# Optimization experiments

Measured on AMD Instinct MI355X. Metric: run time of the kernel, lower is better.

## Reference

```python
import jax, jax.numpy as jnp
import numpy as np

B, A, E, H = 512, 4, 10, 256
OBS, PHY, G, MV = 2, 3, 3, 2
T = 10
STEP = 0.05


def setup_inputs() -> dict:
    key = jax.random.key(0)
    ks = jax.random.split(key, 16)
    rn = lambda k, s, sc=1.0: jax.random.normal(k, s, jnp.float32) * sc
    W = 0.1  # weight scale so tanh/sigmoid stay in sane range
    return {
        'observations': rn(ks[0], (B, A, E, OBS)),
        'physical': rn(ks[1], (B, E, PHY)),
        'observed_goals': rn(ks[2], (B, A, G)),
        'mem_physical': jnp.zeros((B, A, E, H), jnp.float32),
        'mem_action': jnp.zeros((B, A, H), jnp.float32),
        'W_ih_p': rn(ks[3], (3 * H, OBS + PHY), W),
        'W_hh_p': rn(ks[4], (3 * H, H), W),
        'b_ih_p': jnp.zeros((3 * H,), jnp.float32),
        'b_hh_p': jnp.zeros((3 * H,), jnp.float32),
        'W_fc_p': rn(ks[5], (H, H), W),
        'b_fc_p': jnp.zeros((H,), jnp.float32),
        'W_ih_a': rn(ks[6], (3 * H, H + G), W),
        'W_hh_a': rn(ks[7], (3 * H, H), W),
        'b_ih_a': jnp.zeros((3 * H,), jnp.float32),
        'b_hh_a': jnp.zeros((3 * H,), jnp.float32),
        'W_fc_a': rn(ks[8], (H, H), W),
        'b_fc_a': jnp.zeros((H,), jnp.float32),
        'W_m1': rn(ks[9], (H, H), W),
        'b_m1': jnp.zeros((H,), jnp.float32),
        'W_m2': rn(ks[10], (MV, H), W),
        'b_m2': jnp.zeros((MV,), jnp.float32),
    }


def _gru(x, h, Wih, Whh, bih, bhh):
    # torch.nn.GRUCell math, vectorized over leading dims
    gi = x @ Wih.T + bih
    gh = h @ Whh.T + bhh
    ir, iz, inn = jnp.split(gi, 3, axis=-1)
    hr, hz, hn = jnp.split(gh, 3, axis=-1)
    r = jax.nn.sigmoid(ir + hr)
    z = jax.nn.sigmoid(iz + hz)
    n = jnp.tanh(inn + r * hn)
    return (1.0 - z) * n + z * h


def reference(observations, physical, observed_goals, mem_physical, mem_action,
              W_ih_p, W_hh_p, b_ih_p, b_hh_p, W_fc_p, b_fc_p,
              W_ih_a, W_hh_a, b_ih_a, b_hh_a, W_fc_a, b_fc_a,
              W_m1, b_m1, W_m2, b_m2):
    b, a, e, _ = observations.shape
    # per-(agent, entity) input: cat(observation, entity physical features)
    phys_b = jnp.broadcast_to(physical[:, None], (b, a, e, physical.shape[-1]))
    x_p = jnp.concatenate([observations, phys_b], axis=-1)  # [B,A,E,5]

    def step(carry, _):
        mp, ma = carry  # [B,A,E,H], [B,A,H]
        # physical ProcessingModule over all (agent, entity) pairs at once
        h_p = _gru(x_p, mp, W_ih_p, W_hh_p, b_ih_p, b_hh_p)          # new 'physical' memory
        proc = jax.nn.elu(h_p @ W_fc_p.T + b_fc_p)                    # [B,A,E,H]
        feat = jnp.max(proc, axis=2)                                  # AdaptiveMaxPool2d((1,H)) over entities
        # ActionModule: GRU over cat(pooled physical feat, observed goal)
        x_a = jnp.concatenate([feat, observed_goals], axis=-1)       # [B,A,H+G]
        h_a = _gru(x_a, ma, W_ih_a, W_hh_a, b_ih_a, b_hh_a)          # new 'action' memory
        proc_a = jax.nn.elu(h_a @ W_fc_a.T + b_fc_a)
        mv = jnp.tanh(jax.nn.elu(proc_a @ W_m1.T + b_m1) @ W_m2.T + b_m2) * STEP  # [B,A,MV]
        return (h_p, h_a), mv

    _, movements = jax.lax.scan(step, (mem_physical, mem_action), None, length=T)
    return movements  # [T,B,A,MV]
```

## Files before the change

kernel.cpp:

```cpp
#include <hip/hip_runtime.h>
#include <math.h>

#define H 256
#define G3 768
#define BB 512
#define AA 4
#define EE 10
#define RP (BB*AA*EE)
#define RA (BB*AA)
#define TT 10
#define NMV 2
#define STEPSC 0.05f
#define DST 260
#define A1B 128
#define A2B 256
#define A3B 128
#define COMB 1280

typedef __attribute__((ext_vector_type(8))) short short8;
typedef __attribute__((ext_vector_type(8))) _Float16 half8;
typedef __attribute__((ext_vector_type(4))) _Float16 half4;
typedef __attribute__((ext_vector_type(4))) float f32x4;

#if defined(__has_builtin)
#  if __has_builtin(__builtin_amdgcn_global_load_lds)
#    define HAS_GLL 1
#  endif
#endif

__device__ __forceinline__ float sigmoid_(float x){ return 1.f/(1.f + __expf(-x)); }
__device__ __forceinline__ float tanh_(float x){
    float ax = fabsf(x);
    float e  = __expf(-2.f*ax);
    float t  = (1.f - e)/(1.f + e);
    return copysignf(t, x);
}
__device__ __forceinline__ float elu_(float x){ return x > 0.f ? x : (__expf(x) - 1.f); }

#define MFMA16(A,B,C) __builtin_amdgcn_mfma_f32_16x16x32_f16(A,B,C,0,0,0)

__device__ __forceinline__ void cp16(const void* g, void* l) {
#ifdef HAS_GLL
    __builtin_amdgcn_global_load_lds(
        (const __attribute__((address_space(1))) unsigned int*)g,
        (__attribute__((address_space(3))) unsigned int*)l, 16, 0, 0);
#else
    *(short8*)l = *(const short8*)g;
#endif
}

__global__ void k_splitw(const float* __restrict__ src, _Float16* __restrict__ dst,
                         int n, int ldsrc)
{
    int i = blockIdx.x*256 + threadIdx.x;
    if (i < n) {
        int j  = i & 7;
        int l  = (i >> 3) & 63;
        int kc = (i >> 9) & 7;
        int c  = i >> 12;
        int row = c*16 + (l & 15);
        int k   = kc*32 + (l >> 4)*8 + j;
        dst[i] = (_Float16)src[(size_t)row*ldsrc + k];
    }
}

__global__ void k_gia_goal(const float* __restrict__ goals,
                           const float* __restrict__ Wiha,
                           const float* __restrict__ biha,
                           const float* __restrict__ bhha,
                           _Float16* __restrict__ out)
{
    int idx = blockIdx.x*256 + threadIdx.x;
    int ra = idx / G3, k = idx % G3;
    float g0 = goals[ra*3+0], g1 = goals[ra*3+1], g2 = goals[ra*3+2];
    const float* w = Wiha + (size_t)k*259 + 256;
    float base = biha[k] + (k < 512 ? bhha[k] : 0.f);
    out[idx] = (_Float16)(base + g0*w[0] + g1*w[1] + g2*w[2]);
}

__global__ void k_cvt(const float* __restrict__ src, _Float16* __restrict__ dst, int n)
{
    int i = blockIdx.x*256 + threadIdx.x;
    if (i < n) dst[i] = (_Float16)src[i];
}

__global__ void k_xext(const float* __restrict__ obs, const float* __restrict__ phys,
                       _Float16* __restrict__ dst)
{
    int i = blockIdx.x*256 + threadIdx.x;
    int row = i >> 5, j = i & 31;
    float v = 0.f;
    if (j < 2) v = obs[(size_t)row*2 + j];
    else if (j < 5) {
        int bb = row / (AA*EE), e = row % EE;
        v = phys[(size_t)(bb*EE + e)*3 + (j - 2)];
    } else if (j == 5) v = 1.f;
    dst[i] = (_Float16)v;
}

__global__ void k_wxih(const float* __restrict__ Wih, const float* __restrict__ bih,
                       const float* __restrict__ bhh, _Float16* __restrict__ dst)
{
    int i = blockIdx.x*256 + threadIdx.x;
    int j = i & 7, l = (i >> 3) & 63, chunk = i >> 9;
    int g = chunk >> 4, cs = chunk & 15;
    int ocol = g*256 + cs*16 + (l & 15);
    int k32 = (l >> 4)*8 + j;
    float v = 0.f;
    if (k32 < 5) v = Wih[(size_t)ocol*5 + k32];
    else if (k32 == 5) v = bih[ocol] + (g < 2 ? bhh[ocol] : 0.f);
    dst[i] = (_Float16)v;
}

__global__ __launch_bounds__(256, 2)
void k_step(int gru_t, int fc_t, int a1_t, int a2_t, int a3_t,
            _Float16* __restrict__ hp0, _Float16* __restrict__ hp1,
            _Float16* __restrict__ proc0, _Float16* __restrict__ proc1,
            _Float16* __restrict__ ha0, _Float16* __restrict__ ha1,
            _Float16* __restrict__ pca0, _Float16* __restrict__ pca1,
            const _Float16* __restrict__ wWhh, const _Float16* __restrict__ wWfc,
            const _Float16* __restrict__ wWhha, const _Float16* __restrict__ wWiha,
            const _Float16* __restrict__ wWfca, const _Float16* __restrict__ wWm1,
            const _Float16* __restrict__ gia,
            const _Float16* __restrict__ xext, const _Float16* __restrict__ wXih,
            const float* __restrict__ bhh, const float* __restrict__ bfcp,
            const float* __restrict__ bhha, const float* __restrict__ bfca,
            const float* __restrict__ bm1,
            const float* __restrict__ Wm2, const float* __restrict__ bm2,
            float* __restrict__ out)
{
    __shared__ char smem[24576];
    int b = blockIdx.x;
    const int tid = threadIdx.x;
    const int wv = tid >> 6, lane = tid & 63;
    const int quad = lane >> 4, l16 = lane & 15;

    if (b < A1B) {
        if (a1_t < 0) return;
        float* D = (float*)smem;
        const _Float16* proc = (a1_t & 1) ? proc1 : proc0;
        const _Float16* hain = (a1_t & 1) ? ha1 : ha0;
        _Float16*      haout = (a1_t & 1) ? ha0 : ha1;
        const int ra0 = b*16;

        for (int i = tid; i < 16*32; i += 256) {
            int r = i >> 5, cg = (i & 31)*8;
            const _Float16* p = proc + ((size_t)(ra0 + r)*EE)*H + cg;
            half8 v = *(const half8*)p;
            float m[8];
            #pragma unroll
            for (int j = 0; j < 8; j++) m[j] = (float)v[j];
            #pragma unroll
            for (int e = 1; e < EE; e++) {
                half8 u = *(const half8*)(p + (size_t)e*H);
                #pragma unroll
                for (int j = 0; j < 8; j++) m[j] = fmaxf(m[j], (float)u[j]);
            }
            #pragma unroll
            for (int j = 0; j < 8; j++) D[r*DST + cg + j] = m[j];
        }
        __syncthreads();

        half8 Fh[8], Hh[8];
        #pragma unroll
        for (int kc = 0; kc < 8; kc++) {
            const float* fp = &D[l16*DST + quad*8 + kc*32];
            #pragma unroll
            for (int j = 0; j < 8; j++) Fh[kc][j] = (_Float16)fp[j];
            Hh[kc] = *(const half8*)(hain + (size_t)(ra0 + l16)*H + quad*8 + kc*32);
        }

        const int smp = ra0 + l16;
        const _Float16* gp = gia + (size_t)smp*G3;
        #pragma unroll
        for (int p = 0; p < 2; p++) {
            f32x4 gh[3][2], gx[3][2];
            #pragma unroll
            for (int g = 0; g < 3; g++)
                #pragma unroll
                for (int ch = 0; ch < 2; ch++) {
                    gh[g][ch] = (f32x4){0.f,0.f,0.f,0.f};
                    gx[g][ch] = (f32x4){0.f,0.f,0.f,0.f};
                }
            #pragma unroll
            for (int kc = 0; kc < 8; kc++)
                #pragma unroll
                for (int ch = 0; ch < 2; ch++)
                    #pragma unroll
                    for (int g = 0; g < 3; g++) {
                        const size_t cg = (size_t)(g*16 + wv*4 + p*2 + ch);
                        half8 bh = *(const half8*)(wWhha + (cg*8+kc)*512 + lane*8);
                        half8 bx = *(const half8*)(wWiha + (cg*8+kc)*512 + lane*8);
                        gh[g][ch] = MFMA16(bh, Hh[kc], gh[g][ch]);
                        gx[g][ch] = MFMA16(bx, Fh[kc], gx[g][ch]);
                    }
            #pragma unroll
            for (int ch = 0; ch < 2; ch++) {
                const int c0 = (wv*4 + p*2 + ch)*16 + quad*4;
                half4 gr4 = *(const half4*)(gp + c0);
                half4 gz4 = *(const half4*)(gp + 256 + c0);
                half4 gn4 = *(const half4*)(gp + 512 + c0);
                f32x4 bn4 = *(const f32x4*)&bhha[512 + c0];
                half4 hp4 = *(const half4*)(hain + (size_t)smp*H + c0);
                half4 ho;
                #pragma unroll
                for (int r = 0; r < 4; r++) {
                    float rg = sigmoid_((float)gr4[r] + gx[0][ch][r] + gh[0][ch][r]);
                    float z  = sigmoid_((float)gz4[r] + gx[1][ch][r] + gh[1][ch][r]);
                    float n  = tanh_((float)gn4[r] + gx[2][ch][r] + rg*(gh[2][ch][r] + bn4[r]));
                    ho[r] = (_Float16)((1.f - z)*n + z*(float)hp4[r]);
                }
                *(half4*)(haout + (size_t)smp*H + c0) = ho;
            }
        }
        return;
    }
    b -= A1B;

    if (b < A2B) {
        if (a2_t < 0) return;
        const _Float16* hnew = (a2_t & 1) ? ha0 : ha1;
        _Float16*       pca  = (a2_t & 1) ? pca1 : pca0;
        const int ra0 = (b >> 1)*16;
        const int half = b & 1;

        half8 Hh[8];
        #pragma unroll
        for (int kc = 0; kc < 8; kc++)
            Hh[kc] = *(const half8*)(hnew + (size_t)(ra0 + l16)*H + quad*8 + kc*32);

        f32x4 ac[2];
        ac[0] = (f32x4){0.f,0.f,0.f,0.f};
        ac[1] = (f32x4){0.f,0.f,0.f,0.f};
        #pragma unroll
        for (int kc = 0; kc < 8; kc++)
            #pragma unroll
            for (int ch = 0; ch < 2; ch++) {
                const size_t cidx = (size_t)(half*8 + wv*2 + ch);
                half8 w = *(const half8*)(wWfca + (cidx*8+kc)*512 + lane*8);
                ac[ch] = MFMA16(w, Hh[kc], ac[ch]);
            }
        const int smp = ra0 + l16;
        #pragma unroll
        for (int ch = 0; ch < 2; ch++) {
            const int c0 = (half*8 + wv*2 + ch)*16 + quad*4;
            f32x4 bs4 = *(const f32x4*)&bfca[c0];
            half4 po;
            #pragma unroll
            for (int r = 0; r < 4; r++)
                po[r] = (_Float16)elu_(ac[ch][r] + bs4[r]);
            *(half4*)(pca + (size_t)smp*H + c0) = po;
        }
        return;
    }
    b -= A2B;

    if (b < A3B) {
        if (a3_t < 0) return;
        float* D = (float*)smem;
        const _Float16* pca = (a3_t & 1) ? pca1 : pca0;
        const int ra0 = b*16;

        half8 Ph[8];
        #pragma unroll
        for (int kc = 0; kc < 8; kc++)
            Ph[kc] = *(const half8*)(pca + (size_t)(ra0 + l16)*H + quad*8 + kc*32);

        f32x4 ac[4];
        #pragma unroll
        for (int ch = 0; ch < 4; ch++) ac[ch] = (f32x4){0.f,0.f,0.f,0.f};
        #pragma unroll
        for (int kc = 0; kc < 8; kc++)
            #pragma unroll
            for (int ch = 0; ch < 4; ch++) {
                half8 w = *(const half8*)(wWm1 + ((size_t)(wv*4+ch)*8+kc)*512 + lane*8);
                ac[ch] = MFMA16(w, Ph[kc], ac[ch]);
            }
        #pragma unroll
        for (int ch = 0; ch < 4; ch++) {
            const int c0 = (wv*4 + ch)*16 + quad*4;
            f32x4 bs4 = *(const f32x4*)&bm1[c0];
            f32x4 dv;
            #pragma unroll
            for (int r = 0; r < 4; r++) dv[r] = elu_(ac[ch][r] + bs4[r]);
            *(f32x4*)&D[l16*DST + c0] = dv;
        }
        __syncthreads();

        if (tid < 32) {
            int r = tid >> 1, v = tid & 1;
            const float* w = Wm2 + (size_t)v*H;
            float s = bm2[v];
            #pragma unroll 4
            for (int i = 0; i < H/4; i++) {
                float4 a = *(const float4*)&D[r*DST + i*4];
                float4 c = *(const float4*)&w[i*4];
                s = fmaf(a.x,c.x,s); s = fmaf(a.y,c.y,s);
                s = fmaf(a.z,c.z,s); s = fmaf(a.w,c.w,s);
            }
            out[((size_t)a3_t*RA + ra0 + r)*NMV + v] = tanh_(s)*STEPSC;
        }
        return;
    }
    b -= A3B;

    {
        const bool do_gru = (gru_t >= 0);
        const bool do_fc  = (fc_t >= 0);
        if (!do_gru && !do_fc) return;
        _Float16* Bw = (_Float16*)smem;
        const int par = do_gru ? (gru_t & 1) : ((fc_t + 1) & 1);
        const _Float16* hin  = par ? hp1 : hp0;
        _Float16*       hout = par ? hp0 : hp1;
        _Float16*       pout = (fc_t & 1) ? proc1 : proc0;
        const int xm = b % 160, ys = b / 160;
        const int mt0 = xm*128 + wv*16;
        const int mt1 = mt0 + 64;

        half8 Ah[2][8];
        #pragma unroll
        for (int kc = 0; kc < 8; kc++) {
            Ah[0][kc] = *(const half8*)(hin + (size_t)(mt0 + l16)*H + quad*8 + kc*32);
            Ah[1][kc] = *(const half8*)(hin + (size_t)(mt1 + l16)*H + quad*8 + kc*32);
        }

        if (do_gru) {
            half8 Xh[2];
            Xh[0] = *(const half8*)(xext + (size_t)(mt0 + l16)*32 + quad*8);
            Xh[1] = *(const half8*)(xext + (size_t)(mt1 + l16)*32 + quad*8);

            for (int s = 0; s < 2; s++) {
                const int cs = ys*2 + s;
                if (s) __syncthreads();
                #pragma unroll
                for (int k = 0; k < 6; k++) {
                    int i = tid + 256*k;
                    int g = i >> 9;
                    cp16(wWhh + (size_t)(g*16+cs)*4096 + (i & 511)*8, &Bw[(size_t)i*8]);
                }
                __syncthreads();

                f32x4 acc[2][3], accHN[2];
                #pragma unroll
                for (int mt = 0; mt < 2; mt++) {
                    #pragma unroll
                    for (int g = 0; g < 3; g++) acc[mt][g] = (f32x4){0.f,0.f,0.f,0.f};
                    accHN[mt] = (f32x4){0.f,0.f,0.f,0.f};
                }
                #pragma unroll
                for (int kc = 0; kc < 8; kc++) {
                    #pragma unroll
                    for (int g = 0; g < 2; g++) {
                        half8 w = *(const half8*)&Bw[(g*8 + kc)*512 + lane*8];
                        acc[0][g] = MFMA16(w, Ah[0][kc], acc[0][g]);
                        acc[1][g] = MFMA16(w, Ah[1][kc], acc[1][g]);
                    }
                    half8 wn = *(const half8*)&Bw[(2*8 + kc)*512 + lane*8];
                    accHN[0] = MFMA16(wn, Ah[0][kc], accHN[0]);
                    accHN[1] = MFMA16(wn, Ah[1][kc], accHN[1]);
                }
                #pragma unroll
                for (int g = 0; g < 3; g++) {
                    half8 xw = *(const half8*)(wXih + (size_t)(g*16+cs)*512 + lane*8);
                    acc[0][g] = MFMA16(xw, Xh[0], acc[0][g]);
                    acc[1][g] = MFMA16(xw, Xh[1], acc[1][g]);
                }

                const int c0 = cs*16 + quad*4;
                f32x4 bn4 = *(const f32x4*)&bhh[512 + c0];
                #pragma unroll
                for (int mt = 0; mt < 2; mt++) {
                    const int smp = (mt ? mt1 : mt0) + l16;
                    half4 hp4 = *(const half4*)(hin + (size_t)smp*H + c0);
                    half4 ho;
                    #pragma unroll
                    for (int r = 0; r < 4; r++) {
                        float rg = sigmoid_(acc[mt][0][r]);
                        float z  = sigmoid_(acc[mt][1][r]);
                        float n  = tanh_(acc[mt][2][r] + rg*(accHN[mt][r] + bn4[r]));
                        ho[r] = (_Float16)((1.f - z)*n + z*(float)hp4[r]);
                    }
                    *(half4*)(hout + (size_t)smp*H + c0) = ho;
                }
            }
        }

        if (do_fc) {
            const int cs2 = ys;
            __syncthreads();
            #pragma unroll
            for (int k = 0; k < 4; k++) {
                int i = tid + 256*k;
                cp16(wWfc + (size_t)cs2*8192 + i*8, &Bw[(size_t)i*8]);
            }
            __syncthreads();

            f32x4 acc[2][2];
            #pragma unroll
            for (int mt = 0; mt < 2; mt++)
                #pragma unroll
                for (int ni = 0; ni < 2; ni++) acc[mt][ni] = (f32x4){0.f,0.f,0.f,0.f};
            #pragma unroll
            for (int kc = 0; kc < 8; kc++)
                #pragma unroll
                for (int ni = 0; ni < 2; ni++) {
                    half8 w = *(const half8*)&Bw[ni*4096 + kc*512 + lane*8];
                    acc[0][ni] = MFMA16(w, Ah[0][kc], acc[0][ni]);
                    acc[1][ni] = MFMA16(w, Ah[1][kc], acc[1][ni]);
                }
            #pragma unroll
            for (int ni = 0; ni < 2; ni++) {
                const int c0 = cs2*32 + ni*16 + quad*4;
                f32x4 bs4 = *(const f32x4*)&bfcp[c0];
                #pragma unroll
                for (int mt = 0; mt < 2; mt++) {
                    const int smp = (mt ? mt1 : mt0) + l16;
                    half4 po;
                    #pragma unroll
                    for (int r = 0; r < 4; r++)
                        po[r] = (_Float16)elu_(acc[mt][ni][r] + bs4[r]);
                    *(half4*)(pout + (size_t)smp*H + c0) = po;
                }
            }
        }
    }
}

extern "C" void kernel_launch(void* const* d_in, const int* in_sizes, int n_in,
                              void* d_out, int out_size, void* d_ws, size_t ws_size,
                              hipStream_t stream)
{
    const float* obs  = (const float*)d_in[0];
    const float* phys = (const float*)d_in[1];
    const float* goals= (const float*)d_in[2];
    const float* memp = (const float*)d_in[3];
    const float* mema = (const float*)d_in[4];
    const float* Wihp = (const float*)d_in[5];
    const float* Whhp = (const float*)d_in[6];
    const float* bihp = (const float*)d_in[7];
    const float* bhhp = (const float*)d_in[8];
    const float* Wfcp = (const float*)d_in[9];
    const float* bfcp = (const float*)d_in[10];
    const float* Wiha = (const float*)d_in[11];
    const float* Whha = (const float*)d_in[12];
    const float* biha = (const float*)d_in[13];
    const float* bhha = (const float*)d_in[14];
    const float* Wfca = (const float*)d_in[15];
    const float* bfca = (const float*)d_in[16];
    const float* Wm1  = (const float*)d_in[17];
    const float* bm1  = (const float*)d_in[18];
    const float* Wm2  = (const float*)d_in[19];
    const float* bm2  = (const float*)d_in[20];
    float* out = (float*)d_out;
    (void)ws_size;

    char* base = (char*)d_ws;
    size_t off = 0;
    auto alloc = [&](size_t bytes) -> char* {
        char* p = base + off;
        off += (bytes + 255) & ~(size_t)255;
        return p;
    };
    _Float16* wp_whh = (_Float16*)alloc((size_t)G3*H*2);
    _Float16* wp_wfc = (_Float16*)alloc((size_t)H*H*2);
    _Float16* wa_whh = (_Float16*)alloc((size_t)G3*H*2);
    _Float16* wa_wih = (_Float16*)alloc((size_t)G3*H*2);
    _Float16* wa_wfc = (_Float16*)alloc((size_t)H*H*2);
    _Float16* wa_wm1 = (_Float16*)alloc((size_t)H*H*2);
    _Float16* gia    = (_Float16*)alloc((size_t)RA*G3*2);
    _Float16* hp0    = (_Float16*)alloc((size_t)RP*H*2);
    _Float16* hp1    = (_Float16*)alloc((size_t)RP*H*2);
    _Float16* proc0  = (_Float16*)alloc((size_t)RP*H*2);
    _Float16* proc1  = (_Float16*)alloc((size_t)RP*H*2);
    _Float16* ha0    = (_Float16*)alloc((size_t)RA*H*2);
    _Float16* ha1    = (_Float16*)alloc((size_t)RA*H*2);
    _Float16* pca0   = (_Float16*)alloc((size_t)RA*H*2);
    _Float16* pca1   = (_Float16*)alloc((size_t)RA*H*2);
    _Float16* xext   = (_Float16*)alloc((size_t)RP*32*2);
    _Float16* wxih   = (_Float16*)alloc((size_t)48*512*2);

    k_splitw<<<(G3*H+255)/256, 256, 0, stream>>>(Whhp, wp_whh, G3*H, H);
    k_splitw<<<(H*H+255)/256, 256, 0, stream>>>(Wfcp, wp_wfc, H*H, H);
    k_splitw<<<(G3*H+255)/256, 256, 0, stream>>>(Whha, wa_whh, G3*H, H);
    k_splitw<<<(G3*H+255)/256, 256, 0, stream>>>(Wiha, wa_wih, G3*H, 259);
    k_splitw<<<(H*H+255)/256, 256, 0, stream>>>(Wfca, wa_wfc, H*H, H);
    k_splitw<<<(H*H+255)/256, 256, 0, stream>>>(Wm1,  wa_wm1, H*H, H);
    k_gia_goal<<<RA*G3/256, 256, 0, stream>>>(goals, Wiha, biha, bhha, gia);
    k_cvt<<<((size_t)RP*H+255)/256, 256, 0, stream>>>(memp, hp0, RP*H);
    k_cvt<<<((size_t)RA*H+255)/256, 256, 0, stream>>>(mema, ha0, RA*H);
    k_xext<<<RP*32/256, 256, 0, stream>>>(obs, phys, xext);
    k_wxih<<<48*512/256, 256, 0, stream>>>(Wihp, bihp, bhhp, wxih);

    const int NB = A1B + A2B + A3B + COMB;
    for (int L = 0; L <= TT + 3; L++) {
        int gru_t = (L <= TT-1) ? L : -1;
        int fc_t  = (L-1 >= 0 && L-1 <= TT-1) ? L-1 : -1;
        int a1_t  = (L-2 >= 0 && L-2 <= TT-1) ? L-2 : -1;
        int a2_t  = (L-3 >= 0 && L-3 <= TT-1) ? L-3 : -1;
        int a3_t  = (L-4 >= 0 && L-4 <= TT-1) ? L-4 : -1;
        k_step<<<NB, 256, 0, stream>>>(gru_t, fc_t, a1_t, a2_t, a3_t,
                                       hp0, hp1, proc0, proc1, ha0, ha1, pca0, pca1,
                                       wp_whh, wp_wfc, wa_whh, wa_wih, wa_wfc, wa_wm1,
                                       gia, xext, wxih,
                                       bhhp, bfcp,
                                       bhha, bfca, bm1, Wm2, bm2, out);
    }
}
```

Baseline: 599.0 us.

## Read GRU/FC weights straight from global memory and schedule heavy blocks first

The combined physical GRU+FC blocks no longer stage weight tiles into LDS with global_load_lds and barriers. Each wave now loads its MFMA B-fragments directly from global memory, relying on L1/L2 caching. Those heavy COMB blocks also move to the front of the grid so they dispatch before the lighter action-module blocks, and the shared memory size shrinks. The trade-off is more redundant global/L2 traffic per wave in exchange for removing the copy and sync overhead and possibly improving occupancy.

```diff
diff --git a/kernel.cpp b/kernel.cpp
--- a/kernel.cpp
+++ b/kernel.cpp
@@ -22,12 +22,6 @@
 typedef __attribute__((ext_vector_type(4))) _Float16 half4;
 typedef __attribute__((ext_vector_type(4))) float f32x4;
 
-#if defined(__has_builtin)
-#  if __has_builtin(__builtin_amdgcn_global_load_lds)
-#    define HAS_GLL 1
-#  endif
-#endif
-
 __device__ __forceinline__ float sigmoid_(float x){ return 1.f/(1.f + __expf(-x)); }
 __device__ __forceinline__ float tanh_(float x){
     float ax = fabsf(x);
@@ -38,16 +32,6 @@
 __device__ __forceinline__ float elu_(float x){ return x > 0.f ? x : (__expf(x) - 1.f); }
 
 #define MFMA16(A,B,C) __builtin_amdgcn_mfma_f32_16x16x32_f16(A,B,C,0,0,0)
-
-__device__ __forceinline__ void cp16(const void* g, void* l) {
-#ifdef HAS_GLL
-    __builtin_amdgcn_global_load_lds(
-        (const __attribute__((address_space(1))) unsigned int*)g,
-        (__attribute__((address_space(3))) unsigned int*)l, 16, 0, 0);
-#else
-    *(short8*)l = *(const short8*)g;
-#endif
-}
 
 __global__ void k_splitw(const float* __restrict__ src, _Float16* __restrict__ dst,
                          int n, int ldsrc)
@@ -129,186 +113,16 @@
             const float* __restrict__ Wm2, const float* __restrict__ bm2,
             float* __restrict__ out)
 {
-    __shared__ char smem[24576];
+    __shared__ char smem[16640];
     int b = blockIdx.x;
     const int tid = threadIdx.x;
     const int wv = tid >> 6, lane = tid & 63;
     const int quad = lane >> 4, l16 = lane & 15;
 
-    if (b < A1B) {
-        if (a1_t < 0) return;
-        float* D = (float*)smem;
-        const _Float16* proc = (a1_t & 1) ? proc1 : proc0;
-        const _Float16* hain = (a1_t & 1) ? ha1 : ha0;
-        _Float16*      haout = (a1_t & 1) ? ha0 : ha1;
-        const int ra0 = b*16;
-
-        for (int i = tid; i < 16*32; i += 256) {
-            int r = i >> 5, cg = (i & 31)*8;
-            const _Float16* p = proc + ((size_t)(ra0 + r)*EE)*H + cg;
-            half8 v = *(const half8*)p;
-            float m[8];
-            #pragma unroll
-            for (int j = 0; j < 8; j++) m[j] = (float)v[j];
-            #pragma unroll
-            for (int e = 1; e < EE; e++) {
-                half8 u = *(const half8*)(p + (size_t)e*H);
-                #pragma unroll
-                for (int j = 0; j < 8; j++) m[j] = fmaxf(m[j], (float)u[j]);
-            }
-            #pragma unroll
-            for (int j = 0; j < 8; j++) D[r*DST + cg + j] = m[j];
-        }
-        __syncthreads();
-
-        half8 Fh[8], Hh[8];
-        #pragma unroll
-        for (int kc = 0; kc < 8; kc++) {
-            const float* fp = &D[l16*DST + quad*8 + kc*32];
-            #pragma unroll
-            for (int j = 0; j < 8; j++) Fh[kc][j] = (_Float16)fp[j];
-            Hh[kc] = *(const half8*)(hain + (size_t)(ra0 + l16)*H + quad*8 + kc*32);
-        }
-
-        const int smp = ra0 + l16;
-        const _Float16* gp = gia + (size_t)smp*G3;
-        #pragma unroll
-        for (int p = 0; p < 2; p++) {
-            f32x4 gh[3][2], gx[3][2];
-            #pragma unroll
-            for (int g = 0; g < 3; g++)
-                #pragma unroll
-                for (int ch = 0; ch < 2; ch++) {
-                    gh[g][ch] = (f32x4){0.f,0.f,0.f,0.f};
-                    gx[g][ch] = (f32x4){0.f,0.f,0.f,0.f};
-                }
-            #pragma unroll
-            for (int kc = 0; kc < 8; kc++)
-                #pragma unroll
-                for (int ch = 0; ch < 2; ch++)
-                    #pragma unroll
-                    for (int g = 0; g < 3; g++) {
-                        const size_t cg = (size_t)(g*16 + wv*4 + p*2 + ch);
-                        half8 bh = *(const half8*)(wWhha + (cg*8+kc)*512 + lane*8);
-                        half8 bx = *(const half8*)(wWiha + (cg*8+kc)*512 + lane*8);
-                        gh[g][ch] = MFMA16(bh, Hh[kc], gh[g][ch]);
-                        gx[g][ch] = MFMA16(bx, Fh[kc], gx[g][ch]);
-                    }
-            #pragma unroll
-            for (int ch = 0; ch < 2; ch++) {
-                const int c0 = (wv*4 + p*2 + ch)*16 + quad*4;
-                half4 gr4 = *(const half4*)(gp + c0);
-                half4 gz4 = *(const half4*)(gp + 256 + c0);
-                half4 gn4 = *(const half4*)(gp + 512 + c0);
-                f32x4 bn4 = *(const f32x4*)&bhha[512 + c0];
-                half4 hp4 = *(const half4*)(hain + (size_t)smp*H + c0);
-                half4 ho;
-                #pragma unroll
-                for (int r = 0; r < 4; r++) {
-                    float rg = sigmoid_((float)gr4[r] + gx[0][ch][r] + gh[0][ch][r]);
-                    float z  = sigmoid_((float)gz4[r] + gx[1][ch][r] + gh[1][ch][r]);
-                    float n  = tanh_((float)gn4[r] + gx[2][ch][r] + rg*(gh[2][ch][r] + bn4[r]));
-                    ho[r] = (_Float16)((1.f - z)*n + z*(float)hp4[r]);
-                }
-                *(half4*)(haout + (size_t)smp*H + c0) = ho;
-            }
-        }
-        return;
-    }
-    b -= A1B;
-
-    if (b < A2B) {
-        if (a2_t < 0) return;
-        const _Float16* hnew = (a2_t & 1) ? ha0 : ha1;
-        _Float16*       pca  = (a2_t & 1) ? pca1 : pca0;
-        const int ra0 = (b >> 1)*16;
-        const int half = b & 1;
-
-        half8 Hh[8];
-        #pragma unroll
-        for (int kc = 0; kc < 8; kc++)
-            Hh[kc] = *(const half8*)(hnew + (size_t)(ra0 + l16)*H + quad*8 + kc*32);
-
-        f32x4 ac[2];
-        ac[0] = (f32x4){0.f,0.f,0.f,0.f};
-        ac[1] = (f32x4){0.f,0.f,0.f,0.f};
-        #pragma unroll
-        for (int kc = 0; kc < 8; kc++)
-            #pragma unroll
-            for (int ch = 0; ch < 2; ch++) {
-                const size_t cidx = (size_t)(half*8 + wv*2 + ch);
-                half8 w = *(const half8*)(wWfca + (cidx*8+kc)*512 + lane*8);
-                ac[ch] = MFMA16(w, Hh[kc], ac[ch]);
-            }
-        const int smp = ra0 + l16;
-        #pragma unroll
-        for (int ch = 0; ch < 2; ch++) {
-            const int c0 = (half*8 + wv*2 + ch)*16 + quad*4;
-            f32x4 bs4 = *(const f32x4*)&bfca[c0];
-            half4 po;
-            #pragma unroll
-            for (int r = 0; r < 4; r++)
-                po[r] = (_Float16)elu_(ac[ch][r] + bs4[r]);
-            *(half4*)(pca + (size_t)smp*H + c0) = po;
-        }
-        return;
-    }
-    b -= A2B;
-
-    if (b < A3B) {
-        if (a3_t < 0) return;
-        float* D = (float*)smem;
-        const _Float16* pca = (a3_t & 1) ? pca1 : pca0;
-        const int ra0 = b*16;
-
-        half8 Ph[8];
-        #pragma unroll
-        for (int kc = 0; kc < 8; kc++)
-            Ph[kc] = *(const half8*)(pca + (size_t)(ra0 + l16)*H + quad*8 + kc*32);
-
-        f32x4 ac[4];
-        #pragma unroll
-        for (int ch = 0; ch < 4; ch++) ac[ch] = (f32x4){0.f,0.f,0.f,0.f};
-        #pragma unroll
-        for (int kc = 0; kc < 8; kc++)
-            #pragma unroll
-            for (int ch = 0; ch < 4; ch++) {
-                half8 w = *(const half8*)(wWm1 + ((size_t)(wv*4+ch)*8+kc)*512 + lane*8);
-                ac[ch] = MFMA16(w, Ph[kc], ac[ch]);
-            }
-        #pragma unroll
-        for (int ch = 0; ch < 4; ch++) {
-            const int c0 = (wv*4 + ch)*16 + quad*4;
-            f32x4 bs4 = *(const f32x4*)&bm1[c0];
-            f32x4 dv;
-            #pragma unroll
-            for (int r = 0; r < 4; r++) dv[r] = elu_(ac[ch][r] + bs4[r]);
-            *(f32x4*)&D[l16*DST + c0] = dv;
-        }
-        __syncthreads();
-
-        if (tid < 32) {
-            int r = tid >> 1, v = tid & 1;
-            const float* w = Wm2 + (size_t)v*H;
-            float s = bm2[v];
-            #pragma unroll 4
-            for (int i = 0; i < H/4; i++) {
-                float4 a = *(const float4*)&D[r*DST + i*4];
-                float4 c = *(const float4*)&w[i*4];
-                s = fmaf(a.x,c.x,s); s = fmaf(a.y,c.y,s);
-                s = fmaf(a.z,c.z,s); s = fmaf(a.w,c.w,s);
-            }
-            out[((size_t)a3_t*RA + ra0 + r)*NMV + v] = tanh_(s)*STEPSC;
-        }
-        return;
-    }
-    b -= A3B;
-
-    {
+    if (b < COMB) {
         const bool do_gru = (gru_t >= 0);
         const bool do_fc  = (fc_t >= 0);
         if (!do_gru && !do_fc) return;
-        _Float16* Bw = (_Float16*)smem;
         const int par = do_gru ? (gru_t & 1) : ((fc_t + 1) & 1);
         const _Float16* hin  = par ? hp1 : hp0;
         _Float16*       hout = par ? hp0 : hp1;
@@ -329,16 +143,10 @@
             Xh[0] = *(const half8*)(xext + (size_t)(mt0 + l16)*32 + quad*8);
             Xh[1] = *(const half8*)(xext + (size_t)(mt1 + l16)*32 + quad*8);
 
+            #pragma unroll
             for (int s = 0; s < 2; s++) {
                 const int cs = ys*2 + s;
-                if (s) __syncthreads();
-                #pragma unroll
-                for (int k = 0; k < 6; k++) {
-                    int i = tid + 256*k;
-                    int g = i >> 9;
-                    cp16(wWhh + (size_t)(g*16+cs)*4096 + (i & 511)*8, &Bw[(size_t)i*8]);
-                }
-                __syncthreads();
+                const _Float16* wb = wWhh + (size_t)cs*4096 + (size_t)lane*8;
 
                 f32x4 acc[2][3], accHN[2];
                 #pragma unroll
@@ -351,11 +159,11 @@
                 for (int kc = 0; kc < 8; kc++) {
                     #pragma unroll
                     for (int g = 0; g < 2; g++) {
-                        half8 w = *(const half8*)&Bw[(g*8 + kc)*512 + lane*8];
+                        half8 w = *(const half8*)(wb + (size_t)g*65536 + kc*512);
                         acc[0][g] = MFMA16(w, Ah[0][kc], acc[0][g]);
                         acc[1][g] = MFMA16(w, Ah[1][kc], acc[1][g]);
                     }
-                    half8 wn = *(const half8*)&Bw[(2*8 + kc)*512 + lane*8];
+                    half8 wn = *(const half8*)(wb + (size_t)2*65536 + kc*512);
                     accHN[0] = MFMA16(wn, Ah[0][kc], accHN[0]);
                     accHN[1] = MFMA16(wn, Ah[1][kc], accHN[1]);
                 }
@@ -387,14 +195,7 @@
 
         if (do_fc) {
             const int cs2 = ys;
-            __syncthreads();
-            #pragma unroll
-            for (int k = 0; k < 4; k++) {
-                int i = tid + 256*k;
-                cp16(wWfc + (size_t)cs2*8192 + i*8, &Bw[(size_t)i*8]);
-            }
-            __syncthreads();
-
+            const _Float16* wf = wWfc + (size_t)cs2*8192 + (size_t)lane*8;
             f32x4 acc[2][2];
             #pragma unroll
             for (int mt = 0; mt < 2; mt++)
@@ -404,7 +205,7 @@
             for (int kc = 0; kc < 8; kc++)
                 #pragma unroll
                 for (int ni = 0; ni < 2; ni++) {
-                    half8 w = *(const half8*)&Bw[ni*4096 + kc*512 + lane*8];
+                    half8 w = *(const half8*)(wf + ni*4096 + kc*512);
                     acc[0][ni] = MFMA16(w, Ah[0][kc], acc[0][ni]);
                     acc[1][ni] = MFMA16(w, Ah[1][kc], acc[1][ni]);
                 }
@@ -423,6 +224,176 @@
                 }
             }
         }
+        return;
+    }
+    b -= COMB;
+
+    if (b < A1B) {
+        if (a1_t < 0) return;
+        float* D = (float*)smem;
+        const _Float16* proc = (a1_t & 1) ? proc1 : proc0;
+        const _Float16* hain = (a1_t & 1) ? ha1 : ha0;
+        _Float16*      haout = (a1_t & 1) ? ha0 : ha1;
+        const int ra0 = b*16;
+
+        for (int i = tid; i < 16*32; i += 256) {
+            int r = i >> 5, cg = (i & 31)*8;
+            const _Float16* p = proc + ((size_t)(ra0 + r)*EE)*H + cg;
+            half8 v = *(const half8*)p;
+            float m[8];
+            #pragma unroll
+            for (int j = 0; j < 8; j++) m[j] = (float)v[j];
+            #pragma unroll
+            for (int e = 1; e < EE; e++) {
+                half8 u = *(const half8*)(p + (size_t)e*H);
+                #pragma unroll
+                for (int j = 0; j < 8; j++) m[j] = fmaxf(m[j], (float)u[j]);
+            }
+            #pragma unroll
+            for (int j = 0; j < 8; j++) D[r*DST + cg + j] = m[j];
+        }
+        __syncthreads();
+
+        half8 Fh[8], Hh[8];
+        #pragma unroll
+        for (int kc = 0; kc < 8; kc++) {
+            const float* fp = &D[l16*DST + quad*8 + kc*32];
+            #pragma unroll
+            for (int j = 0; j < 8; j++) Fh[kc][j] = (_Float16)fp[j];
+            Hh[kc] = *(const half8*)(hain + (size_t)(ra0 + l16)*H + quad*8 + kc*32);
+        }
+
+        const int smp = ra0 + l16;
+        const _Float16* gp = gia + (size_t)smp*G3;
+        #pragma unroll
+        for (int p = 0; p < 2; p++) {
+            f32x4 gh[3][2], gx[3][2];
+            #pragma unroll
+            for (int g = 0; g < 3; g++)
+                #pragma unroll
+                for (int ch = 0; ch < 2; ch++) {
+                    gh[g][ch] = (f32x4){0.f,0.f,0.f,0.f};
+                    gx[g][ch] = (f32x4){0.f,0.f,0.f,0.f};
+                }
+            #pragma unroll
+            for (int kc = 0; kc < 8; kc++)
+                #pragma unroll
+                for (int ch = 0; ch < 2; ch++)
+                    #pragma unroll
+                    for (int g = 0; g < 3; g++) {
+                        const size_t cg = (size_t)(g*16 + wv*4 + p*2 + ch);
+                        half8 bh = *(const half8*)(wWhha + (cg*8+kc)*512 + lane*8);
+                        half8 bx = *(const half8*)(wWiha + (cg*8+kc)*512 + lane*8);
+                        gh[g][ch] = MFMA16(bh, Hh[kc], gh[g][ch]);
+                        gx[g][ch] = MFMA16(bx, Fh[kc], gx[g][ch]);
+                    }
+            #pragma unroll
+            for (int ch = 0; ch < 2; ch++) {
+                const int c0 = (wv*4 + p*2 + ch)*16 + quad*4;
+                half4 gr4 = *(const half4*)(gp + c0);
+                half4 gz4 = *(const half4*)(gp + 256 + c0);
+                half4 gn4 = *(const half4*)(gp + 512 + c0);
+                f32x4 bn4 = *(const f32x4*)&bhha[512 + c0];
+                half4 hp4 = *(const half4*)(hain + (size_t)smp*H + c0);
+                half4 ho;
+                #pragma unroll
+                for (int r = 0; r < 4; r++) {
+                    float rg = sigmoid_((float)gr4[r] + gx[0][ch][r] + gh[0][ch][r]);
+                    float z  = sigmoid_((float)gz4[r] + gx[1][ch][r] + gh[1][ch][r]);
+                    float n  = tanh_((float)gn4[r] + gx[2][ch][r] + rg*(gh[2][ch][r] + bn4[r]));
+                    ho[r] = (_Float16)((1.f - z)*n + z*(float)hp4[r]);
+                }
+                *(half4*)(haout + (size_t)smp*H + c0) = ho;
+            }
+        }
+        return;
+    }
+    b -= A1B;
+
+    if (b < A2B) {
+        if (a2_t < 0) return;
+        const _Float16* hnew = (a2_t & 1) ? ha0 : ha1;
+        _Float16*       pca  = (a2_t & 1) ? pca1 : pca0;
+        const int ra0 = (b >> 1)*16;
+        const int half = b & 1;
+
+        half8 Hh[8];
+        #pragma unroll
+        for (int kc = 0; kc < 8; kc++)
+            Hh[kc] = *(const half8*)(hnew + (size_t)(ra0 + l16)*H + quad*8 + kc*32);
+
+        f32x4 ac[2];
+        ac[0] = (f32x4){0.f,0.f,0.f,0.f};
+        ac[1] = (f32x4){0.f,0.f,0.f,0.f};
+        #pragma unroll
+        for (int kc = 0; kc < 8; kc++)
+            #pragma unroll
+            for (int ch = 0; ch < 2; ch++) {
+                const size_t cidx = (size_t)(half*8 + wv*2 + ch);
+                half8 w = *(const half8*)(wWfca + (cidx*8+kc)*512 + lane*8);
+                ac[ch] = MFMA16(w, Hh[kc], ac[ch]);
+            }
+        const int smp = ra0 + l16;
+        #pragma unroll
+        for (int ch = 0; ch < 2; ch++) {
+            const int c0 = (half*8 + wv*2 + ch)*16 + quad*4;
+            f32x4 bs4 = *(const f32x4*)&bfca[c0];
+            half4 po;
+            #pragma unroll
+            for (int r = 0; r < 4; r++)
+                po[r] = (_Float16)elu_(ac[ch][r] + bs4[r]);
+            *(half4*)(pca + (size_t)smp*H + c0) = po;
+        }
+        return;
+    }
+    b -= A2B;
+
+    if (b < A3B) {
+        if (a3_t < 0) return;
+        float* D = (float*)smem;
+        const _Float16* pca = (a3_t & 1) ? pca1 : pca0;
+        const int ra0 = b*16;
+
+        half8 Ph[8];
+        #pragma unroll
+        for (int kc = 0; kc < 8; kc++)
+            Ph[kc] = *(const half8*)(pca + (size_t)(ra0 + l16)*H + quad*8 + kc*32);
+
+        f32x4 ac[4];
+        #pragma unroll
+        for (int ch = 0; ch < 4; ch++) ac[ch] = (f32x4){0.f,0.f,0.f,0.f};
+        #pragma unroll
+        for (int kc = 0; kc < 8; kc++)
+            #pragma unroll
+            for (int ch = 0; ch < 4; ch++) {
+                half8 w = *(const half8*)(wWm1 + ((size_t)(wv*4+ch)*8+kc)*512 + lane*8);
+                ac[ch] = MFMA16(w, Ph[kc], ac[ch]);
+            }
+        #pragma unroll
+        for (int ch = 0; ch < 4; ch++) {
+            const int c0 = (wv*4 + ch)*16 + quad*4;
+            f32x4 bs4 = *(const f32x4*)&bm1[c0];
+            f32x4 dv;
+            #pragma unroll
+            for (int r = 0; r < 4; r++) dv[r] = elu_(ac[ch][r] + bs4[r]);
+            *(f32x4*)&D[l16*DST + c0] = dv;
+        }
+        __syncthreads();
+
+        if (tid < 32) {
+            int r = tid >> 1, v = tid & 1;
+            const float* w = Wm2 + (size_t)v*H;
+            float s = bm2[v];
+            #pragma unroll 4
+            for (int i = 0; i < H/4; i++) {
+                float4 a = *(const float4*)&D[r*DST + i*4];
+                float4 c = *(const float4*)&w[i*4];
+                s = fmaf(a.x,c.x,s); s = fmaf(a.y,c.y,s);
+                s = fmaf(a.z,c.z,s); s = fmaf(a.w,c.w,s);
+            }
+            out[((size_t)a3_t*RA + ra0 + r)*NMV + v] = tanh_(s)*STEPSC;
+        }
+        return;
     }
 }
 
@@ -491,7 +462,7 @@
     k_xext<<<RP*32/256, 256, 0, stream>>>(obs, phys, xext);
     k_wxih<<<48*512/256, 256, 0, stream>>>(Wihp, bihp, bhhp, wxih);
 
-    const int NB = A1B + A2B + A3B + COMB;
+    const int NB = COMB + A1B + A2B + A3B;
     for (int L = 0; L <= TT + 3; L++) {
         int gru_t = (L <= TT-1) ? L : -1;
         int fc_t  = (L-1 >= 0 && L-1 <= TT-1) ? L-1 : -1;
```

After: 758.5 us. 26.6% more time.
